# Optimization experiments

Measured on AMD Instinct MI355X. Metric: run time of the kernel, lower is better.

## Reference

```python
import jax, jax.numpy as jnp
import numpy as np

B, IN, H, OUT = 8192, 2048, 2048, 512
DEG = 4            # polynomial_degree -> DEG+1 basis functions
BN_EPS = 1e-5


def setup_inputs() -> dict:
    key = jax.random.key(0)
    ks = jax.random.split(key, 8)
    inv_in = 1.0 / np.sqrt(IN)
    inv_h = 1.0 / np.sqrt(H)
    inv_deg = 1.0 / (IN * (DEG + 1))
    return {
        "x": jax.random.normal(ks[0], (B, IN), jnp.float32),
        "w1_base": jax.random.normal(ks[1], (H, IN), jnp.float32) * inv_in,
        "b1_base": jnp.zeros((H,), jnp.float32),
        "c1": jax.random.normal(ks[2], (IN, H, DEG + 1), jnp.float32) * inv_deg,
        "s1": jnp.ones((H,), jnp.float32),
        "bn_gamma": jnp.ones((H,), jnp.float32),
        "bn_beta": jnp.zeros((H,), jnp.float32),
        "w2_base": jax.random.normal(ks[3], (OUT, H), jnp.float32) * inv_h,
        "b2_base": jnp.zeros((OUT,), jnp.float32),
        "c2": jax.random.normal(ks[4], (H, OUT, DEG + 1), jnp.float32) * (1.0 / (H * (DEG + 1))),
        "s2": jnp.ones((OUT,), jnp.float32),
    }


def _cheby_kan_linear(x, w_base, b_base, coeffs, scaler):
    # Base linear path (skip_activation=True -> no SiLU on x).
    base = x @ w_base.T + b_base                      # [B, out]
    # tanh normalization into [-1, 1] for Chebyshev domain.
    xn = jnp.tanh(x)                                  # [B, in]
    Ts = [jnp.ones_like(xn), xn]
    for _ in range(DEG - 1):
        Ts.append(2.0 * xn * Ts[-1] - Ts[-2])
    T = jnp.stack(Ts, axis=-1)                        # [B, in, DEG+1]
    poly = jnp.einsum('bid,iod->bo', T, coeffs)       # [B, out]
    return base + poly * scaler


def _batchnorm1d(x, gamma, beta):
    # Training-mode BatchNorm1d: biased batch statistics over the batch axis.
    mu = jnp.mean(x, axis=0)
    var = jnp.var(x, axis=0)
    return gamma * (x - mu) * jax.lax.rsqrt(var + BN_EPS) + beta


def reference(x, w1_base, b1_base, c1, s1, bn_gamma, bn_beta,
              w2_base, b2_base, c2, s2):
    h = _cheby_kan_linear(x, w1_base, b1_base, c1, s1)
    h = _batchnorm1d(h, bn_gamma, bn_beta)
    return _cheby_kan_linear(h, w2_base, b2_base, c2, s2)
```

## Files before the change

### kernel.cpp

```cpp
#include <hip/hip_runtime.h>
#include <hip/hip_bf16.h>

#define NB   8192
#define NI   2048
#define NH   2048
#define NO   512
#define KP   10240
#define CHNK 4096
#define BNEPS 1e-5f

typedef short bf16x8 __attribute__((ext_vector_type(8)));
typedef float f32x4 __attribute__((ext_vector_type(4)));
typedef unsigned int u32_g __attribute__((address_space(1)));
typedef unsigned int u32_l __attribute__((address_space(3)));

__device__ __forceinline__ void load_lds16(const void* g, void* l) {
  __builtin_amdgcn_global_load_lds((const u32_g*)g, (u32_l*)l, 16, 0, 0);
}

__device__ __forceinline__ unsigned short f2bf(float f) {
  __hip_bfloat16 h = __float2bfloat16(f);
  unsigned short u;
  __builtin_memcpy(&u, &h, 2);
  return u;
}

__global__ __launch_bounds__(256) void build_w_kernel(
    const float* __restrict__ wbase, const float* __restrict__ coef,
    const float* __restrict__ scaler, __hip_bfloat16* __restrict__ Wp,
    float* __restrict__ acc, int Nout, int Kin)
{
  __shared__ float lds0[64][65];
  __shared__ __hip_bfloat16 ldsT[64][4][68];
  const int t = threadIdx.x;
  const int o0 = blockIdx.x * 64;
  const int i0 = blockIdx.y * 64;

  for (int r = t; r < 64 * 64 * 5; r += 256) {
    int li = r / 320;
    int rem = r - li * 320;
    int lo = rem / 5;
    int d = rem - lo * 5;
    float v = coef[((size_t)(i0 + li) * Nout + (o0 + lo)) * 5 + d];
    if (d == 0) lds0[lo][li] = v;
    else        ldsT[lo][d - 1][li] = __float2bfloat16(v);
  }
  __syncthreads();

  const size_t Kw = (size_t)5 * Kin;
  for (int r = t; r < 64 * 4 * 64; r += 256) {
    int li = r & 63;
    int d  = (r >> 6) & 3;
    int lo = r >> 8;
    float v = __bfloat162float(ldsT[lo][d][li]) * scaler[o0 + lo];
    Wp[(size_t)(o0 + lo) * Kw + (size_t)(d + 1) * Kin + i0 + li] = __float2bfloat16(v);
  }
  for (int r = t; r < 64 * 64; r += 256) {
    int li = r & 63;
    int lo = r >> 6;
    Wp[(size_t)(o0 + lo) * Kw + i0 + li] =
        __float2bfloat16(wbase[(size_t)(o0 + lo) * Kin + i0 + li]);
  }
  {
    int lo = t >> 2, q = t & 3;
    float s = 0.f;
    #pragma unroll
    for (int j = 0; j < 16; ++j) s += lds0[lo][q * 16 + j];
    s += __shfl_xor(s, 1);
    s += __shfl_xor(s, 2);
    if (q == 0) atomicAdd(&acc[o0 + lo], s);
  }
}

__global__ __launch_bounds__(256) void build_a1_kernel(
    const float* __restrict__ x, __hip_bfloat16* __restrict__ Ap, int b0)
{
  const size_t idx = ((size_t)blockIdx.x * 256 + threadIdx.x) * 4;
  const size_t row = idx >> 11;
  const int i = (int)(idx & 2047);
  const float4 xv = *(const float4*)(x + (size_t)b0 * NI + idx);
  const float xa[4] = {xv.x, xv.y, xv.z, xv.w};
  unsigned short u0[4], u1[4], u2[4], u3[4], u4[4];
  #pragma unroll
  for (int j = 0; j < 4; ++j) {
    float v  = xa[j];
    float tn = tanhf(v);
    float t2 = fmaf(2.f * tn, tn, -1.f);
    float t3 = fmaf(2.f * tn, t2, -tn);
    float t4 = fmaf(2.f * tn, t3, -t2);
    u0[j] = f2bf(v);  u1[j] = f2bf(tn); u2[j] = f2bf(t2);
    u3[j] = f2bf(t3); u4[j] = f2bf(t4);
  }
  __hip_bfloat16* bp = Ap + row * KP + i;
  *(ushort4*)(bp)          = make_ushort4(u0[0], u0[1], u0[2], u0[3]);
  *(ushort4*)(bp + NI)     = make_ushort4(u1[0], u1[1], u1[2], u1[3]);
  *(ushort4*)(bp + 2 * NI) = make_ushort4(u2[0], u2[1], u2[2], u2[3]);
  *(ushort4*)(bp + 3 * NI) = make_ushort4(u3[0], u3[1], u3[2], u3[3]);
  *(ushort4*)(bp + 4 * NI) = make_ushort4(u4[0], u4[1], u4[2], u4[3]);
}

__global__ __launch_bounds__(256) void build_a2_kernel(
    const __hip_bfloat16* __restrict__ h, const float* __restrict__ mu,
    const float* __restrict__ rsig, const float* __restrict__ gam,
    const float* __restrict__ bet, __hip_bfloat16* __restrict__ Ap, int b0)
{
  const size_t idx = ((size_t)blockIdx.x * 256 + threadIdx.x) * 4;
  const size_t row = idx >> 11;
  const int j0 = (int)(idx & 2047);
  const ushort4 hv = *(const ushort4*)(h + (size_t)b0 * NH + idx);
  const float4 muv = *(const float4*)(mu + j0);
  const float4 rsv = *(const float4*)(rsig + j0);
  const float4 gv  = *(const float4*)(gam + j0);
  const float4 bv  = *(const float4*)(bet + j0);
  unsigned short hu[4] = {hv.x, hv.y, hv.z, hv.w};
  const float ma[4] = {muv.x, muv.y, muv.z, muv.w};
  const float ra[4] = {rsv.x, rsv.y, rsv.z, rsv.w};
  const float ga[4] = {gv.x, gv.y, gv.z, gv.w};
  const float ba[4] = {bv.x, bv.y, bv.z, bv.w};
  unsigned short u0[4], u1[4], u2[4], u3[4], u4[4];
  #pragma unroll
  for (int j = 0; j < 4; ++j) {
    __hip_bfloat16 hb;
    __builtin_memcpy(&hb, &hu[j], 2);
    float hv_f = __bfloat162float(hb);
    float hn = fmaf(ga[j] * (hv_f - ma[j]), ra[j], ba[j]);
    float tn = tanhf(hn);
    float t2 = fmaf(2.f * tn, tn, -1.f);
    float t3 = fmaf(2.f * tn, t2, -tn);
    float t4 = fmaf(2.f * tn, t3, -t2);
    u0[j] = f2bf(hn); u1[j] = f2bf(tn); u2[j] = f2bf(t2);
    u3[j] = f2bf(t3); u4[j] = f2bf(t4);
  }
  __hip_bfloat16* bp = Ap + row * KP + j0;
  *(ushort4*)(bp)          = make_ushort4(u0[0], u0[1], u0[2], u0[3]);
  *(ushort4*)(bp + NH)     = make_ushort4(u1[0], u1[1], u1[2], u1[3]);
  *(ushort4*)(bp + 2 * NH) = make_ushort4(u2[0], u2[1], u2[2], u2[3]);
  *(ushort4*)(bp + 3 * NH) = make_ushort4(u3[0], u3[1], u3[2], u3[3]);
  *(ushort4*)(bp + 4 * NH) = make_ushort4(u4[0], u4[1], u4[2], u4[3]);
}

__global__ __launch_bounds__(256) void bn_stats_kernel(
    const __hip_bfloat16* __restrict__ h, float* __restrict__ psum,
    float* __restrict__ psq)
{
  const int col = blockIdx.x * 256 + threadIdx.x;
  const int r0 = blockIdx.y * 256;
  float s = 0.f, q = 0.f;
  for (int r = 0; r < 256; ++r) {
    float v = __bfloat162float(h[(size_t)(r0 + r) * NH + col]);
    s += v;
    q = fmaf(v, v, q);
  }
  psum[(size_t)blockIdx.y * NH + col] = s;
  psq [(size_t)blockIdx.y * NH + col] = q;
}

__global__ __launch_bounds__(256) void bn_finalize_kernel(
    const float* __restrict__ psum, const float* __restrict__ psq,
    float* __restrict__ mu, float* __restrict__ rsig)
{
  const int j = blockIdx.x * 256 + threadIdx.x;
  float s = 0.f, q = 0.f;
  for (int c = 0; c < 32; ++c) {
    s += psum[(size_t)c * NH + j];
    q += psq [(size_t)c * NH + j];
  }
  const float invB = 1.f / (float)NB;
  float m = s * invB;
  float var = fmaf(q, invB, -m * m);
  mu[j] = m;
  rsig[j] = rsqrtf(var + BNEPS);
}

__global__ __launch_bounds__(256) void bias_init_kernel(
    float* __restrict__ out, const float* __restrict__ bb,
    const float* __restrict__ bs, const float* __restrict__ bacc)
{
  const size_t idx = ((size_t)blockIdx.x * 256 + threadIdx.x) * 4;
  const int col = (int)(idx & (NO - 1));
  const float4 b = *(const float4*)(bb + col);
  const float4 s = *(const float4*)(bs + col);
  const float4 a = *(const float4*)(bacc + col);
  float4 o;
  o.x = b.x + s.x * a.x; o.y = b.y + s.y * a.y;
  o.z = b.z + s.z * a.z; o.w = b.w + s.w * a.w;
  *(float4*)(out + idx) = o;
}

template<int MF>
__global__ __launch_bounds__(256) void gemm_bt_h(
    const __hip_bfloat16* __restrict__ A, const __hip_bfloat16* __restrict__ Bm,
    __hip_bfloat16* __restrict__ C, const float* __restrict__ bb,
    const float* __restrict__ bs, const float* __restrict__ bacc,
    int N, int K)
{
  constexpr int BM = MF * 32;
  __shared__ __attribute__((aligned(16))) __hip_bfloat16 As[BM][64];
  __shared__ __attribute__((aligned(16))) __hip_bfloat16 Bs[128][64];
  const int t = threadIdx.x;
  const int lane = t & 63;
  const int w = t >> 6;
  const int swz = ((int)blockIdx.x & 7) * ((int)gridDim.x >> 3) + ((int)blockIdx.x >> 3);
  const int nTN = N >> 7;
  const int m0 = (swz / nTN) * BM;
  const int n0 = (swz % nTN) * 128;
  const int wr = (w >> 1) * (MF * 16);
  const int wc = (w & 1) * 64;
  const int sr = lane >> 3;
  const int sc = (lane & 7) * 8;
  const __hip_bfloat16* Ag = A  + (size_t)(m0 + w * (8 * MF) + sr) * K + sc;
  const __hip_bfloat16* Bg = Bm + (size_t)(n0 + w * 32 + sr) * K + sc;

  f32x4 acc[MF][4];
  #pragma unroll
  for (int m = 0; m < MF; ++m)
    #pragma unroll
    for (int n = 0; n < 4; ++n) {
      f32x4 z = {0.f, 0.f, 0.f, 0.f};
      acc[m][n] = z;
    }

  const int fr = lane & 15;
  const int kg = (lane >> 4) * 8;

  for (int kt = 0; kt < K; kt += 64) {
    #pragma unroll
    for (int c = 0; c < MF; ++c)
      load_lds16(Ag + (size_t)c * 8 * K + kt, &As[w * 8 * MF + c * 8][0]);
    #pragma unroll
    for (int c = 0; c < 4; ++c)
      load_lds16(Bg + (size_t)c * 8 * K + kt, &Bs[w * 32 + c * 8][0]);
    __syncthreads();
    #pragma unroll
    for (int kk = 0; kk < 2; ++kk) {
      bf16x8 af[MF], bfr[4];
      #pragma unroll
      for (int m = 0; m < MF; ++m)
        af[m] = *(const bf16x8*)&As[wr + m * 16 + fr][kk * 32 + kg];
      #pragma unroll
      for (int n = 0; n < 4; ++n)
        bfr[n] = *(const bf16x8*)&Bs[wc + n * 16 + fr][kk * 32 + kg];
      #pragma unroll
      for (int m = 0; m < MF; ++m)
        #pragma unroll
        for (int n = 0; n < 4; ++n)
          acc[m][n] = __builtin_amdgcn_mfma_f32_16x16x32_bf16(
              af[m], bfr[n], acc[m][n], 0, 0, 0);
    }
    __syncthreads();
  }

  const int cr = (lane >> 4) * 4;
  const int cc = lane & 15;
  #pragma unroll
  for (int n = 0; n < 4; ++n) {
    const int col = n0 + wc + n * 16 + cc;
    const float bias = bb[col] + bs[col] * bacc[col];
    #pragma unroll
    for (int m = 0; m < MF; ++m) {
      __hip_bfloat16* Cp = C + (size_t)(m0 + wr + m * 16 + cr) * N + col;
      #pragma unroll
      for (int r = 0; r < 4; ++r)
        Cp[(size_t)r * N] = __float2bfloat16(acc[m][n][r] + bias);
    }
  }
}

template<int MF>
__global__ __launch_bounds__(256) void gemm_bt_atomic(
    const __hip_bfloat16* __restrict__ A, const __hip_bfloat16* __restrict__ Bm,
    float* __restrict__ C, int N, int Kstride, int K2, int lg2bps)
{
  constexpr int BM = MF * 32;
  __shared__ __attribute__((aligned(16))) __hip_bfloat16 As[BM][64];
  __shared__ __attribute__((aligned(16))) __hip_bfloat16 Bs[128][64];
  const int t = threadIdx.x;
  const int lane = t & 63;
  const int w = t >> 6;
  const int swz = ((int)blockIdx.x & 7) * ((int)gridDim.x >> 3) + ((int)blockIdx.x >> 3);
  const int split = swz >> lg2bps;
  const int l = swz & ((1 << lg2bps) - 1);
  const int nTN = N >> 7;
  const int m0 = (l / nTN) * BM;
  const int n0 = (l % nTN) * 128;
  const int k0 = split * K2;
  const int wr = (w >> 1) * (MF * 16);
  const int wc = (w & 1) * 64;
  const int sr = lane >> 3;
  const int sc = (lane & 7) * 8;
  const __hip_bfloat16* Ag = A  + (size_t)(m0 + w * (8 * MF) + sr) * Kstride + sc;
  const __hip_bfloat16* Bg = Bm + (size_t)(n0 + w * 32 + sr) * Kstride + sc;

  f32x4 acc[MF][4];
  #pragma unroll
  for (int m = 0; m < MF; ++m)
    #pragma unroll
    for (int n = 0; n < 4; ++n) {
      f32x4 z = {0.f, 0.f, 0.f, 0.f};
      acc[m][n] = z;
    }

  const int fr = lane & 15;
  const int kg = (lane >> 4) * 8;

  for (int kt = k0; kt < k0 + K2; kt += 64) {
    #pragma unroll
    for (int c = 0; c < MF; ++c)
      load_lds16(Ag + (size_t)c * 8 * Kstride + kt, &As[w * 8 * MF + c * 8][0]);
    #pragma unroll
    for (int c = 0; c < 4; ++c)
      load_lds16(Bg + (size_t)c * 8 * Kstride + kt, &Bs[w * 32 + c * 8][0]);
    __syncthreads();
    #pragma unroll
    for (int kk = 0; kk < 2; ++kk) {
      bf16x8 af[MF], bfr[4];
      #pragma unroll
      for (int m = 0; m < MF; ++m)
        af[m] = *(const bf16x8*)&As[wr + m * 16 + fr][kk * 32 + kg];
      #pragma unroll
      for (int n = 0; n < 4; ++n)
        bfr[n] = *(const bf16x8*)&Bs[wc + n * 16 + fr][kk * 32 + kg];
      #pragma unroll
      for (int m = 0; m < MF; ++m)
        #pragma unroll
        for (int n = 0; n < 4; ++n)
          acc[m][n] = __builtin_amdgcn_mfma_f32_16x16x32_bf16(
              af[m], bfr[n], acc[m][n], 0, 0, 0);
    }
    __syncthreads();
  }

  const int cr = (lane >> 4) * 4;
  const int cc = lane & 15;
  #pragma unroll
  for (int n = 0; n < 4; ++n) {
    const int col = n0 + wc + n * 16 + cc;
    #pragma unroll
    for (int m = 0; m < MF; ++m) {
      float* Cp = C + (size_t)(m0 + wr + m * 16 + cr) * N + col;
      #pragma unroll
      for (int r = 0; r < 4; ++r)
        atomicAdd(&Cp[(size_t)r * N], acc[m][n][r]);
    }
  }
}

extern "C" void kernel_launch(void* const* d_in, const int* in_sizes, int n_in,
                              void* d_out, int out_size, void* d_ws, size_t ws_size,
                              hipStream_t stream) {
  (void)in_sizes; (void)n_in; (void)out_size;
  const float* x   = (const float*)d_in[0];
  const float* w1  = (const float*)d_in[1];
  const float* b1  = (const float*)d_in[2];
  const float* c1  = (const float*)d_in[3];
  const float* s1  = (const float*)d_in[4];
  const float* gam = (const float*)d_in[5];
  const float* bet = (const float*)d_in[6];
  const float* w2  = (const float*)d_in[7];
  const float* b2  = (const float*)d_in[8];
  const float* c2  = (const float*)d_in[9];
  const float* s2  = (const float*)d_in[10];
  float* out = (float*)d_out;

  const bool full = ws_size >= 243820544ULL;
  const size_t apBytes = full ? 167772160ULL : 83886080ULL;
  char* ws = (char*)d_ws;
  __hip_bfloat16* Ap = (__hip_bfloat16*)ws;
  __hip_bfloat16* Wp = (__hip_bfloat16*)(ws + apBytes);
  __hip_bfloat16* hb = (__hip_bfloat16*)(ws + apBytes + 41943040ULL);
  char* tail = ws + apBytes + 41943040ULL + 33554432ULL;
  float* acc1 = (float*)(tail);
  float* acc2 = (float*)(tail + 8192);
  float* psum = (float*)(tail + 10240);
  float* psq  = (float*)(tail + 272384);
  float* mu   = (float*)(tail + 534528);
  float* rsig = (float*)(tail + 542720);

  dim3 blk(256);
  hipMemsetAsync(acc1, 0, 8192 + 2048, stream);

  build_w_kernel<<<dim3(NH / 64, NI / 64), blk, 0, stream>>>(w1, c1, s1, Wp, acc1, NH, NI);

  if (full) {
    build_a1_kernel<<<(NB * NI / 4) / 256, blk, 0, stream>>>(x, Ap, 0);
    gemm_bt_h<4><<<(NB / 128) * (NH / 128), blk, 0, stream>>>(
        Ap, Wp, hb, b1, s1, acc1, NH, KP);
  } else {
    for (int ch = 0; ch < 2; ++ch) {
      int b0 = ch * CHNK;
      build_a1_kernel<<<(CHNK * NI / 4) / 256, blk, 0, stream>>>(x, Ap, b0);
      gemm_bt_h<4><<<(CHNK / 128) * (NH / 128), blk, 0, stream>>>(
          Ap, Wp, hb + (size_t)b0 * NH, b1, s1, acc1, NH, KP);
    }
  }

  bn_stats_kernel<<<dim3(NH / 256, 32), blk, 0, stream>>>(hb, psum, psq);
  bn_finalize_kernel<<<NH / 256, blk, 0, stream>>>(psum, psq, mu, rsig);

  build_w_kernel<<<dim3(NO / 64, NH / 64), blk, 0, stream>>>(w2, c2, s2, Wp, acc2, NO, NH);

  bias_init_kernel<<<(NB * NO / 4) / 256, blk, 0, stream>>>(out, b2, s2, acc2);

  if (full) {
    build_a2_kernel<<<(NB * NH / 4) / 256, blk, 0, stream>>>(hb, mu, rsig, gam, bet, Ap, 0);
    gemm_bt_atomic<4><<<4 * (NB / 128) * (NO / 128), blk, 0, stream>>>(
        Ap, Wp, out, NO, KP, KP / 4, 8);
  } else {
    for (int ch = 0; ch < 2; ++ch) {
      int b0 = ch * CHNK;
      build_a2_kernel<<<(CHNK * NH / 4) / 256, blk, 0, stream>>>(hb, mu, rsig, gam, bet, Ap, b0);
      gemm_bt_atomic<4><<<4 * (CHNK / 128) * (NO / 128), blk, 0, stream>>>(
          Ap, Wp, out + (size_t)b0 * NO, NO, KP, KP / 4, 7);
    }
  }
}
```

Before: 1.110 ms.

## Double-buffer GEMM LDS tiles with XOR swizzle and unified atomic/bias kernel

Both GEMMs move to a single templated kernel that double-buffers the A and B LDS tiles. The next-next k-tile is prefetched through global_load_lds while the MFMAs run on the current one, using explicit vmcnt waits and raw barriers instead of two __syncthreads per iteration. It also XOR-swizzles the LDS column layout to cut bank conflicts, raises MFMA priority with s_setprio, and adds a launch-bounds occupancy hint of 2. The cost is double the LDS per block (64KB), which can limit occupancy, and the waitcnt sequencing is fragile.

Measured after the change: 907.0 us. 1.22x faster.

```diff
diff --git a/kernel.cpp b/kernel.cpp
--- a/kernel.cpp
+++ b/kernel.cpp
@@ -187,33 +187,39 @@
   *(float4*)(out + idx) = o;
 }
 
-template<int MF>
-__global__ __launch_bounds__(256) void gemm_bt_h(
+template<bool ATOMIC>
+__global__ __launch_bounds__(256, 2) void gemm_db(
     const __hip_bfloat16* __restrict__ A, const __hip_bfloat16* __restrict__ Bm,
-    __hip_bfloat16* __restrict__ C, const float* __restrict__ bb,
+    void* __restrict__ Cv, const float* __restrict__ bb,
     const float* __restrict__ bs, const float* __restrict__ bacc,
-    int N, int K)
-{
-  constexpr int BM = MF * 32;
-  __shared__ __attribute__((aligned(16))) __hip_bfloat16 As[BM][64];
-  __shared__ __attribute__((aligned(16))) __hip_bfloat16 Bs[128][64];
-  const int t = threadIdx.x;
-  const int lane = t & 63;
-  const int w = t >> 6;
-  const int swz = ((int)blockIdx.x & 7) * ((int)gridDim.x >> 3) + ((int)blockIdx.x >> 3);
+    int N, int K, int nt, int lg2bps)
+{
+  __shared__ __attribute__((aligned(16))) __hip_bfloat16 As[2][128][64];
+  __shared__ __attribute__((aligned(16))) __hip_bfloat16 Bs[2][128][64];
+  const int tid  = threadIdx.x;
+  const int lane = tid & 63;
+  const int w    = tid >> 6;
+  int swz = ((int)blockIdx.x & 7) * ((int)gridDim.x >> 3) + ((int)blockIdx.x >> 3);
+  int k0 = 0;
+  if constexpr (ATOMIC) {
+    const int split = swz >> lg2bps;
+    swz &= (1 << lg2bps) - 1;
+    k0 = split * (nt * 64);
+  }
   const int nTN = N >> 7;
-  const int m0 = (swz / nTN) * BM;
+  const int m0 = (swz / nTN) * 128;
   const int n0 = (swz % nTN) * 128;
-  const int wr = (w >> 1) * (MF * 16);
+  const int wr = (w >> 1) * 64;
   const int wc = (w & 1) * 64;
-  const int sr = lane >> 3;
-  const int sc = (lane & 7) * 8;
-  const __hip_bfloat16* Ag = A  + (size_t)(m0 + w * (8 * MF) + sr) * K + sc;
-  const __hip_bfloat16* Bg = Bm + (size_t)(n0 + w * 32 + sr) * K + sc;
-
-  f32x4 acc[MF][4];
+
+  const int srow = lane >> 3;
+  const int scol = (((lane & 7) ^ srow) * 8);
+  const __hip_bfloat16* Ag = A  + (size_t)(m0 + w * 32 + srow) * K + k0 + scol;
+  const __hip_bfloat16* Bg = Bm + (size_t)(n0 + w * 32 + srow) * K + k0 + scol;
+
+  f32x4 acc[4][4];
   #pragma unroll
-  for (int m = 0; m < MF; ++m)
+  for (int m = 0; m < 4; ++m)
     #pragma unroll
     for (int n = 0; n < 4; ++n) {
       f32x4 z = {0.f, 0.f, 0.f, 0.f};
@@ -222,125 +228,84 @@
 
   const int fr = lane & 15;
   const int kg = (lane >> 4) * 8;
-
-  for (int kt = 0; kt < K; kt += 64) {
-    #pragma unroll
-    for (int c = 0; c < MF; ++c)
-      load_lds16(Ag + (size_t)c * 8 * K + kt, &As[w * 8 * MF + c * 8][0]);
-    #pragma unroll
-    for (int c = 0; c < 4; ++c)
-      load_lds16(Bg + (size_t)c * 8 * K + kt, &Bs[w * 32 + c * 8][0]);
-    __syncthreads();
-    #pragma unroll
-    for (int kk = 0; kk < 2; ++kk) {
-      bf16x8 af[MF], bfr[4];
-      #pragma unroll
-      for (int m = 0; m < MF; ++m)
-        af[m] = *(const bf16x8*)&As[wr + m * 16 + fr][kk * 32 + kg];
+  const int swz_r = (fr & 7) * 8;
+
+  #define STAGE(buf, kt)                                                     \
+    do {                                                                     \
+      _Pragma("unroll")                                                      \
+      for (int c = 0; c < 4; ++c)                                            \
+        load_lds16(Ag + (size_t)c * 8 * K + (kt), &As[buf][w * 32 + c * 8][0]); \
+      _Pragma("unroll")                                                      \
+      for (int c = 0; c < 4; ++c)                                            \
+        load_lds16(Bg + (size_t)c * 8 * K + (kt), &Bs[buf][w * 32 + c * 8][0]); \
+    } while (0)
+
+  STAGE(0, 0);
+  STAGE(1, 64);
+  asm volatile("s_waitcnt vmcnt(8)" ::: "memory");
+  __builtin_amdgcn_s_barrier();
+
+  for (int it = 0; it < nt; ++it) {
+    const int cur = it & 1;
+    bf16x8 af[4][2], bfr[4][2];
+    #pragma unroll
+    for (int m = 0; m < 4; ++m)
+      #pragma unroll
+      for (int kk = 0; kk < 2; ++kk)
+        af[m][kk] = *(const bf16x8*)&As[cur][wr + m * 16 + fr][(kk * 32 + kg) ^ swz_r];
+    #pragma unroll
+    for (int n = 0; n < 4; ++n)
+      #pragma unroll
+      for (int kk = 0; kk < 2; ++kk)
+        bfr[n][kk] = *(const bf16x8*)&Bs[cur][wc + n * 16 + fr][(kk * 32 + kg) ^ swz_r];
+    asm volatile("s_waitcnt lgkmcnt(0)" ::: "memory");
+    __builtin_amdgcn_s_barrier();
+    const bool pre = (it + 2 < nt);
+    if (pre) STAGE(cur, (it + 2) * 64);
+    __builtin_amdgcn_s_setprio(1);
+    #pragma unroll
+    for (int m = 0; m < 4; ++m)
       #pragma unroll
       for (int n = 0; n < 4; ++n)
-        bfr[n] = *(const bf16x8*)&Bs[wc + n * 16 + fr][kk * 32 + kg];
-      #pragma unroll
-      for (int m = 0; m < MF; ++m)
         #pragma unroll
-        for (int n = 0; n < 4; ++n)
+        for (int kk = 0; kk < 2; ++kk)
           acc[m][n] = __builtin_amdgcn_mfma_f32_16x16x32_bf16(
-              af[m], bfr[n], acc[m][n], 0, 0, 0);
-    }
-    __syncthreads();
-  }
+              af[m][kk], bfr[n][kk], acc[m][n], 0, 0, 0);
+    __builtin_amdgcn_s_setprio(0);
+    if (pre) asm volatile("s_waitcnt vmcnt(8)" ::: "memory");
+    else     asm volatile("s_waitcnt vmcnt(0)" ::: "memory");
+    __builtin_amdgcn_s_barrier();
+  }
+  #undef STAGE
 
   const int cr = (lane >> 4) * 4;
   const int cc = lane & 15;
-  #pragma unroll
-  for (int n = 0; n < 4; ++n) {
-    const int col = n0 + wc + n * 16 + cc;
-    const float bias = bb[col] + bs[col] * bacc[col];
-    #pragma unroll
-    for (int m = 0; m < MF; ++m) {
-      __hip_bfloat16* Cp = C + (size_t)(m0 + wr + m * 16 + cr) * N + col;
-      #pragma unroll
-      for (int r = 0; r < 4; ++r)
-        Cp[(size_t)r * N] = __float2bfloat16(acc[m][n][r] + bias);
-    }
-  }
-}
-
-template<int MF>
-__global__ __launch_bounds__(256) void gemm_bt_atomic(
-    const __hip_bfloat16* __restrict__ A, const __hip_bfloat16* __restrict__ Bm,
-    float* __restrict__ C, int N, int Kstride, int K2, int lg2bps)
-{
-  constexpr int BM = MF * 32;
-  __shared__ __attribute__((aligned(16))) __hip_bfloat16 As[BM][64];
-  __shared__ __attribute__((aligned(16))) __hip_bfloat16 Bs[128][64];
-  const int t = threadIdx.x;
-  const int lane = t & 63;
-  const int w = t >> 6;
-  const int swz = ((int)blockIdx.x & 7) * ((int)gridDim.x >> 3) + ((int)blockIdx.x >> 3);
-  const int split = swz >> lg2bps;
-  const int l = swz & ((1 << lg2bps) - 1);
-  const int nTN = N >> 7;
-  const int m0 = (l / nTN) * BM;
-  const int n0 = (l % nTN) * 128;
-  const int k0 = split * K2;
-  const int wr = (w >> 1) * (MF * 16);
-  const int wc = (w & 1) * 64;
-  const int sr = lane >> 3;
-  const int sc = (lane & 7) * 8;
-  const __hip_bfloat16* Ag = A  + (size_t)(m0 + w * (8 * MF) + sr) * Kstride + sc;
-  const __hip_bfloat16* Bg = Bm + (size_t)(n0 + w * 32 + sr) * Kstride + sc;
-
-  f32x4 acc[MF][4];
-  #pragma unroll
-  for (int m = 0; m < MF; ++m)
+  if constexpr (ATOMIC) {
+    float* C = (float*)Cv;
     #pragma unroll
     for (int n = 0; n < 4; ++n) {
-      f32x4 z = {0.f, 0.f, 0.f, 0.f};
-      acc[m][n] = z;
-    }
-
-  const int fr = lane & 15;
-  const int kg = (lane >> 4) * 8;
-
-  for (int kt = k0; kt < k0 + K2; kt += 64) {
-    #pragma unroll
-    for (int c = 0; c < MF; ++c)
-      load_lds16(Ag + (size_t)c * 8 * Kstride + kt, &As[w * 8 * MF + c * 8][0]);
-    #pragma unroll
-    for (int c = 0; c < 4; ++c)
-      load_lds16(Bg + (size_t)c * 8 * Kstride + kt, &Bs[w * 32 + c * 8][0]);
-    __syncthreads();
-    #pragma unroll
-    for (int kk = 0; kk < 2; ++kk) {
-      bf16x8 af[MF], bfr[4];
-      #pragma unroll
-      for (int m = 0; m < MF; ++m)
-        af[m] = *(const bf16x8*)&As[wr + m * 16 + fr][kk * 32 + kg];
-      #pragma unroll
-      for (int n = 0; n < 4; ++n)
-        bfr[n] = *(const bf16x8*)&Bs[wc + n * 16 + fr][kk * 32 + kg];
-      #pragma unroll
-      for (int m = 0; m < MF; ++m)
+      const int col = n0 + wc + n * 16 + cc;
+      #pragma unroll
+      for (int m = 0; m < 4; ++m) {
+        float* Cp = C + (size_t)(m0 + wr + m * 16 + cr) * N + col;
         #pragma unroll
-        for (int n = 0; n < 4; ++n)
-          acc[m][n] = __builtin_amdgcn_mfma_f32_16x16x32_bf16(
-              af[m], bfr[n], acc[m][n], 0, 0, 0);
-    }
-    __syncthreads();
-  }
-
-  const int cr = (lane >> 4) * 4;
-  const int cc = lane & 15;
-  #pragma unroll
-  for (int n = 0; n < 4; ++n) {
-    const int col = n0 + wc + n * 16 + cc;
-    #pragma unroll
-    for (int m = 0; m < MF; ++m) {
-      float* Cp = C + (size_t)(m0 + wr + m * 16 + cr) * N + col;
-      #pragma unroll
-      for (int r = 0; r < 4; ++r)
-        atomicAdd(&Cp[(size_t)r * N], acc[m][n][r]);
+        for (int r = 0; r < 4; ++r)
+          atomicAdd(&Cp[(size_t)r * N], acc[m][n][r]);
+      }
+    }
+  } else {
+    __hip_bfloat16* C = (__hip_bfloat16*)Cv;
+    #pragma unroll
+    for (int n = 0; n < 4; ++n) {
+      const int col = n0 + wc + n * 16 + cc;
+      const float bias = bb[col] + bs[col] * bacc[col];
+      #pragma unroll
+      for (int m = 0; m < 4; ++m) {
+        __hip_bfloat16* Cp = C + (size_t)(m0 + wr + m * 16 + cr) * N + col;
+        #pragma unroll
+        for (int r = 0; r < 4; ++r)
+          Cp[(size_t)r * N] = __float2bfloat16(acc[m][n][r] + bias);
+      }
     }
   }
 }
@@ -383,14 +348,14 @@
 
   if (full) {
     build_a1_kernel<<<(NB * NI / 4) / 256, blk, 0, stream>>>(x, Ap, 0);
-    gemm_bt_h<4><<<(NB / 128) * (NH / 128), blk, 0, stream>>>(
-        Ap, Wp, hb, b1, s1, acc1, NH, KP);
+    gemm_db<false><<<(NB / 128) * (NH / 128), blk, 0, stream>>>(
+        Ap, Wp, hb, b1, s1, acc1, NH, KP, KP / 64, 0);
   } else {
     for (int ch = 0; ch < 2; ++ch) {
       int b0 = ch * CHNK;
       build_a1_kernel<<<(CHNK * NI / 4) / 256, blk, 0, stream>>>(x, Ap, b0);
-      gemm_bt_h<4><<<(CHNK / 128) * (NH / 128), blk, 0, stream>>>(
-          Ap, Wp, hb + (size_t)b0 * NH, b1, s1, acc1, NH, KP);
+      gemm_db<false><<<(CHNK / 128) * (NH / 128), blk, 0, stream>>>(
+          Ap, Wp, hb + (size_t)b0 * NH, b1, s1, acc1, NH, KP, KP / 64, 0);
     }
   }
 
@@ -403,14 +368,14 @@
 
   if (full) {
     build_a2_kernel<<<(NB * NH / 4) / 256, blk, 0, stream>>>(hb, mu, rsig, gam, bet, Ap, 0);
-    gemm_bt_atomic<4><<<4 * (NB / 128) * (NO / 128), blk, 0, stream>>>(
-        Ap, Wp, out, NO, KP, KP / 4, 8);
+    gemm_db<true><<<4 * (NB / 128) * (NO / 128), blk, 0, stream>>>(
+        Ap, Wp, out, nullptr, nullptr, nullptr, NO, KP, (KP / 4) / 64, 8);
   } else {
     for (int ch = 0; ch < 2; ++ch) {
       int b0 = ch * CHNK;
       build_a2_kernel<<<(CHNK * NH / 4) / 256, blk, 0, stream>>>(hb, mu, rsig, gam, bet, Ap, b0);
-      gemm_bt_atomic<4><<<4 * (CHNK / 128) * (NO / 128), blk, 0, stream>>>(
-          Ap, Wp, out + (size_t)b0 * NO, NO, KP, KP / 4, 7);
-    }
-  }
-}
+      gemm_db<true><<<4 * (CHNK / 128) * (NO / 128), blk, 0, stream>>>(
+          Ap, Wp, out + (size_t)b0 * NO, nullptr, nullptr, nullptr, NO, KP, (KP / 4) / 64, 7);
+    }
+  }
+}
```
